# Optimization experiments

Hardware: AMD Instinct MI355X
Metric: run time of the kernel (lower is better)

The kernel has to match this reference:

```python
import jax, jax.numpy as jnp
import numpy as np

A, B, D, L = 256, 64, 768, 2  # annotators, batch, hidden, num_labels
G1, G2 = 4, 8                 # groups per attribute


def setup_inputs() -> dict:
    key = jax.random.key(0)
    ks = jax.random.split(key, 9)
    s = 1.0 / np.sqrt(D)
    return {
        "pooled": jax.random.normal(ks[0], (B, D), jnp.float32),
        "W1": jax.random.normal(ks[1], (G1, D, D), jnp.float32) * s,
        "b1": jax.random.normal(ks[2], (G1, D), jnp.float32) * s,
        "W2": jax.random.normal(ks[3], (G2, D, D), jnp.float32) * s,
        "b2": jax.random.normal(ks[4], (G2, D), jnp.float32) * s,
        "Wh": jax.random.normal(ks[5], (A, D, L), jnp.float32) * s,
        "bh": jax.random.normal(ks[6], (A, L), jnp.float32) * s,
        "g1_idx": jax.random.randint(ks[7], (A,), 0, G1),
        "g2_idx": jax.random.randint(ks[8], (A,), 0, G2),
    }


def reference(pooled, W1, b1, W2, b2, Wh, bh, g1_idx, g2_idx):
    # Attribute 1: every annotator with the same group shares the transform,
    # so compute once per group then gather (avoids A redundant GEMMs).
    h_g = jnp.einsum('bd,gde->gbe', pooled, W1) + b1[:, None, :]   # [G1, B, D]
    h = h_g[g1_idx]                                                # [A, B, D]
    # Attribute 2: input now differs per annotator -> grouped GEMM via gathered weights.
    h = jnp.einsum('abd,ade->abe', h, W2[g2_idx]) + b2[g2_idx][:, None, :]  # [A, B, D]
    # Per-annotator classification heads.
    logits = jnp.einsum('abd,adl->abl', h, Wh) + bh[:, None, :]    # [A, B, L]
    # Match torch layout: logits[batch, annotator, label]
    return jnp.transpose(logits, (1, 0, 2))                        # [B, A, L]
```

## Files before the change

kernel.cpp:

```cpp
#include <hip/hip_runtime.h>
#include <hip/hip_bf16.h>

#define AN 256
#define BN 64
#define DN 768
#define G1N 4
#define G2N 8
#define KI 24
#define LPAD 776

typedef __attribute__((ext_vector_type(8))) short short8;
typedef __attribute__((ext_vector_type(4))) short bf16x4;
typedef __attribute__((ext_vector_type(4))) float floatx4;

static __device__ __forceinline__ unsigned short f2bf(float f) {
    union { float f; unsigned int u; } v; v.f = f;
    unsigned int r = v.u + 0x7FFF + ((v.u >> 16) & 1);
    return (unsigned short)(r >> 16);
}
static __device__ __forceinline__ float bf2f(short s) {
    union { unsigned int u; float f; } v;
    v.u = ((unsigned int)(unsigned short)s) << 16;
    return v.f;
}

__global__ __launch_bounds__(256) void k_pack(
    const float* __restrict__ Wh, const float* __restrict__ b2,
    const float* __restrict__ bh, const int* __restrict__ g2i,
    unsigned short* __restrict__ Whp, float* __restrict__ bcu,
    int* __restrict__ s2idx)
{
    const int tid = threadIdx.x, a = blockIdx.x;
    __shared__ int g2s[AN];
    __shared__ int ss;
    g2s[tid] = g2i[tid];
    __syncthreads();
    if (tid == 0) {
        int my = g2s[a], s = 0;
        for (int j = 0; j < a; ++j) s += (g2s[j] == my);
        ss = s;
        s2idx[a] = s;
    }
    __syncthreads();
    const int my = g2s[a], s = ss;
    const size_t r0 = (size_t)my * 512 + 2 * s;
    const float* wa = Wh + (size_t)a * (DN * 2);

    #pragma unroll
    for (int i = 0; i < 3; ++i) {
        int e = i * 256 + tid;
        float2 v = *(const float2*)(wa + e * 2);
        Whp[r0 * DN + e]       = f2bf(v.x);
        Whp[(r0 + 1) * DN + e] = f2bf(v.y);
    }

    const int wave = tid >> 6, lane = tid & 63;
    if (wave < 2) {
        const int l = wave;
        const float* b2p = b2 + (size_t)my * DN;
        float sacc = 0.f;
        #pragma unroll
        for (int k = 0; k < 12; ++k) {
            int e = k * 64 + lane;
            sacc += wa[e * 2 + l] * b2p[e];
        }
        #pragma unroll
        for (int off = 1; off < 64; off <<= 1) sacc += __shfl_xor(sacc, off, 64);
        if (lane == 0) bcu[r0 + l] = sacc + bh[a * 2 + l];
    }
}

__global__ __launch_bounds__(256) void k_u(
    const float* __restrict__ W2, const unsigned short* __restrict__ Whp,
    const int* __restrict__ g2i, unsigned short* __restrict__ Wcs)
{
    const int g = blockIdx.y, d0 = blockIdx.x * 16;
    const int tid = threadIdx.x;
    const int n = __syncthreads_count(g2i[tid] == g);
    const int cols = 2 * n;
    const int nct = (cols + 15) >> 4;

    __shared__ unsigned short Bs[16 * LPAD];
    {
        const int srow = tid >> 4, t16 = tid & 15;
        const float* srcr = W2 + ((size_t)g * DN + d0 + srow) * DN;
        unsigned short* dstr = &Bs[srow * LPAD];
        #pragma unroll
        for (int i = 0; i < 12; ++i) {
            int col4 = (i * 16 + t16) * 4;
            float4 v = *(const float4*)(srcr + col4);
            bf16x4 b;
            b[0] = (short)f2bf(v.x); b[1] = (short)f2bf(v.y);
            b[2] = (short)f2bf(v.z); b[3] = (short)f2bf(v.w);
            *(bf16x4*)(dstr + col4) = b;
        }
    }
    __syncthreads();

    const int lane = tid & 63, wave = tid >> 6;
    const int nn = lane & 15, quad = lane >> 4;
    const unsigned short* bsp = &Bs[nn * LPAD + quad * 8];

    for (int ct = wave; ct < nct; ct += 4) {
        const int c = ct * 16 + nn;
        const int cl = (c < cols) ? c : cols - 1;
        const unsigned short* ap = Whp + ((size_t)g * 512 + cl) * DN + quad * 8;
        floatx4 acc = {0, 0, 0, 0};
        #pragma unroll
        for (int kk = 0; kk < KI; ++kk) {
            short8 af = *(const short8*)(ap + kk * 32);
            short8 bf = *(const short8*)(bsp + kk * 32);
            acc = __builtin_amdgcn_mfma_f32_16x16x32_bf16(af, bf, acc, 0, 0, 0);
        }
        #pragma unroll
        for (int r = 0; r < 4; ++r) {
            int cc = ct * 16 + quad * 4 + r;
            if (cc < cols)
                Wcs[((size_t)g * 512 + cc) * DN + d0 + nn] = f2bf(acc[r]);
        }
    }
}

__global__ __launch_bounds__(256) void k_v(
    const float* __restrict__ W1, const unsigned short* __restrict__ Wcs,
    const float* __restrict__ b1, const float* __restrict__ bcu,
    const int* __restrict__ g1i, const int* __restrict__ g2i,
    const int* __restrict__ s2idx,
    unsigned short* __restrict__ Vs, float* __restrict__ sv)
{
    const int g = blockIdx.y, d0 = blockIdx.x * 16;
    const int tid = threadIdx.x;
    __shared__ int g1s[AN];
    __shared__ int lst[AN];
    __shared__ int rpa[AN];
    g1s[tid] = g1i[tid];
    rpa[tid] = g2i[tid] * 512 + 2 * s2idx[tid];
    __syncthreads();
    int p1 = 0;
    const int m1 = g1s[tid];
    for (int a2 = 0; a2 < tid; ++a2) p1 += (g1s[a2] == m1);
    const int n = __syncthreads_count(m1 == g);
    if (m1 == g) lst[p1] = tid;
    const int cols = 2 * n;
    const int nct = (cols + 15) >> 4;

    __shared__ unsigned short Bs[16 * LPAD];
    {
        const int srow = tid >> 4, t16 = tid & 15;
        const float* srcr = W1 + ((size_t)g * DN + d0 + srow) * DN;
        unsigned short* dstr = &Bs[srow * LPAD];
        #pragma unroll
        for (int i = 0; i < 12; ++i) {
            int col4 = (i * 16 + t16) * 4;
            float4 v = *(const float4*)(srcr + col4);
            bf16x4 b;
            b[0] = (short)f2bf(v.x); b[1] = (short)f2bf(v.y);
            b[2] = (short)f2bf(v.z); b[3] = (short)f2bf(v.w);
            *(bf16x4*)(dstr + col4) = b;
        }
    }
    __syncthreads();

    const int lane = tid & 63, wave = tid >> 6;
    const int nn = lane & 15, quad = lane >> 4;
    const unsigned short* bsp = &Bs[nn * LPAD + quad * 8];
    const bool biasw = (blockIdx.x == 0);

    for (int ct = wave; ct < nct; ct += 4) {
        const int c = ct * 16 + nn;
        const int cl = (c < cols) ? c : cols - 1;
        const int a = lst[cl >> 1];
        const int rp = rpa[a] + (cl & 1);
        const unsigned short* ap = Wcs + (size_t)rp * DN + quad * 8;
        floatx4 acc = {0, 0, 0, 0};
        float sacc = 0.f;
        #pragma unroll
        for (int kk = 0; kk < KI; ++kk) {
            short8 af = *(const short8*)(ap + kk * 32);
            if (biasw) {
                const float* b1p = b1 + (size_t)g * DN + kk * 32 + quad * 8;
                float4 c0v = *(const float4*)(b1p);
                float4 c1v = *(const float4*)(b1p + 4);
                sacc += bf2f(af[0]) * c0v.x + bf2f(af[1]) * c0v.y
                      + bf2f(af[2]) * c0v.z + bf2f(af[3]) * c0v.w
                      + bf2f(af[4]) * c1v.x + bf2f(af[5]) * c1v.y
                      + bf2f(af[6]) * c1v.z + bf2f(af[7]) * c1v.w;
            }
            short8 bf = *(const short8*)(bsp + kk * 32);
            acc = __builtin_amdgcn_mfma_f32_16x16x32_bf16(af, bf, acc, 0, 0, 0);
        }
        #pragma unroll
        for (int r = 0; r < 4; ++r) {
            int cc = ct * 16 + quad * 4 + r;
            if (cc < cols)
                Vs[((size_t)g * 512 + cc) * DN + d0 + nn] = f2bf(acc[r]);
        }
        if (biasw) {
            sacc += __shfl_xor(sacc, 16, 64);
            sacc += __shfl_xor(sacc, 32, 64);
            if (quad == 0 && c < cols)
                sv[g * 512 + c] = sacc + bcu[rp];
        }
    }
}

__global__ __launch_bounds__(256) void k_out(
    const float* __restrict__ pooled, const unsigned short* __restrict__ Vs,
    const float* __restrict__ sv, const int* __restrict__ g1i,
    float* __restrict__ out)
{
    const int g = blockIdx.y;
    const int tid = threadIdx.x;
    __shared__ int g1s[AN];
    __shared__ int lst[AN];
    g1s[tid] = g1i[tid];
    __syncthreads();
    int p1 = 0;
    const int m1 = g1s[tid];
    for (int a2 = 0; a2 < tid; ++a2) p1 += (g1s[a2] == m1);
    const int n = __syncthreads_count(m1 == g);
    if (m1 == g) lst[p1] = tid;
    __syncthreads();
    const int cols = 2 * n;
    const int nt0 = blockIdx.x * 16;
    if (nt0 >= cols) return;

    const int lane = tid & 63, wave = tid >> 6;
    const int nn = lane & 15, quad = lane >> 4;

    const int c = nt0 + nn;
    const bool valid = (c < cols);
    const int cl = valid ? c : cols - 1;
    const int a = lst[cl >> 1], l = cl & 1;

    const float* ap = pooled + (size_t)(wave * 16 + nn) * DN + quad * 8;
    const unsigned short* bp = Vs + (size_t)(g * 512 + cl) * DN + quad * 8;

    floatx4 acc = {0, 0, 0, 0};
    #pragma unroll
    for (int kk = 0; kk < KI; ++kk) {
        float4 a0 = *(const float4*)(ap + kk * 32);
        float4 a1 = *(const float4*)(ap + kk * 32 + 4);
        short8 af;
        af[0] = (short)f2bf(a0.x); af[1] = (short)f2bf(a0.y);
        af[2] = (short)f2bf(a0.z); af[3] = (short)f2bf(a0.w);
        af[4] = (short)f2bf(a1.x); af[5] = (short)f2bf(a1.y);
        af[6] = (short)f2bf(a1.z); af[7] = (short)f2bf(a1.w);
        short8 bf = *(const short8*)(bp + kk * 32);
        acc = __builtin_amdgcn_mfma_f32_16x16x32_bf16(af, bf, acc, 0, 0, 0);
    }
    if (valid) {
        const float bv = sv[g * 512 + cl];
        #pragma unroll
        for (int r = 0; r < 4; ++r)
            out[(size_t)(wave * 16 + quad * 4 + r) * (AN * 2) + a * 2 + l] = acc[r] + bv;
    }
}

extern "C" void kernel_launch(void* const* d_in, const int* in_sizes, int n_in,
                              void* d_out, int out_size, void* d_ws, size_t ws_size,
                              hipStream_t stream) {
    const float* pooled = (const float*)d_in[0];
    const float* W1     = (const float*)d_in[1];
    const float* b1     = (const float*)d_in[2];
    const float* W2     = (const float*)d_in[3];
    const float* b2     = (const float*)d_in[4];
    const float* Wh     = (const float*)d_in[5];
    const float* bh     = (const float*)d_in[6];
    const int*   g1i    = (const int*)d_in[7];
    const int*   g2i    = (const int*)d_in[8];
    float* out = (float*)d_out;

    char* ws = (char*)d_ws;
    float* bcu   = (float*)ws;                  ws += (size_t)G2N * 512 * 4;
    float* sv    = (float*)ws;                  ws += (size_t)G1N * 512 * 4;
    int*   s2idx = (int*)ws;                    ws += (size_t)AN * 4;
    unsigned short* Whp = (unsigned short*)ws;  ws += (size_t)G2N * 512 * DN * 2;
    unsigned short* Wcs = (unsigned short*)ws;  ws += (size_t)G2N * 512 * DN * 2;
    unsigned short* Vs  = (unsigned short*)ws;  ws += (size_t)G1N * 512 * DN * 2;

    dim3 blk(256);
    k_pack<<<dim3(AN),        blk, 0, stream>>>(Wh, b2, bh, g2i, Whp, bcu, s2idx);
    k_u   <<<dim3(48, G2N),   blk, 0, stream>>>(W2, Whp, g2i, Wcs);
    k_v   <<<dim3(48, G1N),   blk, 0, stream>>>(W1, Wcs, b1, bcu, g1i, g2i, s2idx, Vs, sv);
    k_out <<<dim3(32, G1N),   blk, 0, stream>>>(pooled, Vs, sv, g1i, out);
}
```

Measured before the change: 138.1 us.

## Fuse four stage kernels into one persistent kernel with grid barriers

Merges the pack, W2-product, W1-product and output kernels into a single persistent kernel of 384 blocks, separated by atomic-counter grid barriers. A small init kernel resets the counters. This removes three inter-kernel launch gaps and drains. In exchange it relies on all blocks being co-resident, and adds spin-wait barrier overhead and idle blocks in the phases with smaller grids.

```diff
diff --git a/kernel.cpp b/kernel.cpp
--- a/kernel.cpp
+++ b/kernel.cpp
@@ -8,6 +8,7 @@
 #define G2N 8
 #define KI 24
 #define LPAD 776
+#define GRID 384
 
 typedef __attribute__((ext_vector_type(8))) short short8;
 typedef __attribute__((ext_vector_type(4))) short bf16x4;
@@ -24,236 +25,230 @@
     return v.f;
 }
 
-__global__ __launch_bounds__(256) void k_pack(
-    const float* __restrict__ Wh, const float* __restrict__ b2,
-    const float* __restrict__ bh, const int* __restrict__ g2i,
-    unsigned short* __restrict__ Whp, float* __restrict__ bcu,
-    int* __restrict__ s2idx)
+static __device__ __forceinline__ void grid_barrier(unsigned* ctr, unsigned target) {
+    __syncthreads();
+    if (threadIdx.x == 0) {
+        __threadfence();
+        atomicAdd(ctr, 1u);
+        while (__hip_atomic_load(ctr, __ATOMIC_RELAXED, __HIP_MEMORY_SCOPE_AGENT) < target)
+            __builtin_amdgcn_s_sleep(2);
+        __threadfence();
+    }
+    __syncthreads();
+}
+
+__global__ __launch_bounds__(64) void k_init(unsigned* __restrict__ ctr) {
+    if (threadIdx.x < 4) ctr[threadIdx.x] = 0u;
+}
+
+__global__ __launch_bounds__(256, 2) void k_fused(
+    const float* __restrict__ pooled, const float* __restrict__ W1,
+    const float* __restrict__ b1, const float* __restrict__ W2,
+    const float* __restrict__ b2, const float* __restrict__ Wh,
+    const float* __restrict__ bh, const int* __restrict__ g1i,
+    const int* __restrict__ g2i,
+    unsigned* __restrict__ ctr, float* __restrict__ bcu,
+    float* __restrict__ sv, int* __restrict__ s2idx,
+    unsigned short* __restrict__ Whp, unsigned short* __restrict__ Wcs,
+    unsigned short* __restrict__ Vs, float* __restrict__ out)
 {
-    const int tid = threadIdx.x, a = blockIdx.x;
-    __shared__ int g2s[AN];
-    __shared__ int ss;
-    g2s[tid] = g2i[tid];
-    __syncthreads();
-    if (tid == 0) {
-        int my = g2s[a], s = 0;
-        for (int j = 0; j < a; ++j) s += (g2s[j] == my);
-        ss = s;
-        s2idx[a] = s;
-    }
-    __syncthreads();
-    const int my = g2s[a], s = ss;
-    const size_t r0 = (size_t)my * 512 + 2 * s;
-    const float* wa = Wh + (size_t)a * (DN * 2);
-
-    #pragma unroll
-    for (int i = 0; i < 3; ++i) {
-        int e = i * 256 + tid;
-        float2 v = *(const float2*)(wa + e * 2);
-        Whp[r0 * DN + e]       = f2bf(v.x);
-        Whp[(r0 + 1) * DN + e] = f2bf(v.y);
-    }
-
-    const int wave = tid >> 6, lane = tid & 63;
-    if (wave < 2) {
-        const int l = wave;
-        const float* b2p = b2 + (size_t)my * DN;
-        float sacc = 0.f;
-        #pragma unroll
-        for (int k = 0; k < 12; ++k) {
-            int e = k * 64 + lane;
-            sacc += wa[e * 2 + l] * b2p[e];
-        }
-        #pragma unroll
-        for (int off = 1; off < 64; off <<= 1) sacc += __shfl_xor(sacc, off, 64);
-        if (lane == 0) bcu[r0 + l] = sacc + bh[a * 2 + l];
-    }
-}
-
-__global__ __launch_bounds__(256) void k_u(
-    const float* __restrict__ W2, const unsigned short* __restrict__ Whp,
-    const int* __restrict__ g2i, unsigned short* __restrict__ Wcs)
-{
-    const int g = blockIdx.y, d0 = blockIdx.x * 16;
+    __shared__ unsigned short Bs[16 * LPAD];
+    __shared__ int arrA[AN];
+    __shared__ int arrB[AN];
+    __shared__ int arrC[AN];
+    __shared__ int sscalar;
+
+    const int bx = blockIdx.x;
     const int tid = threadIdx.x;
-    const int n = __syncthreads_count(g2i[tid] == g);
-    const int cols = 2 * n;
-    const int nct = (cols + 15) >> 4;
-
-    __shared__ unsigned short Bs[16 * LPAD];
-    {
-        const int srow = tid >> 4, t16 = tid & 15;
-        const float* srcr = W2 + ((size_t)g * DN + d0 + srow) * DN;
-        unsigned short* dstr = &Bs[srow * LPAD];
-        #pragma unroll
-        for (int i = 0; i < 12; ++i) {
-            int col4 = (i * 16 + t16) * 4;
-            float4 v = *(const float4*)(srcr + col4);
-            bf16x4 b;
-            b[0] = (short)f2bf(v.x); b[1] = (short)f2bf(v.y);
-            b[2] = (short)f2bf(v.z); b[3] = (short)f2bf(v.w);
-            *(bf16x4*)(dstr + col4) = b;
-        }
-    }
-    __syncthreads();
-
     const int lane = tid & 63, wave = tid >> 6;
     const int nn = lane & 15, quad = lane >> 4;
-    const unsigned short* bsp = &Bs[nn * LPAD + quad * 8];
-
-    for (int ct = wave; ct < nct; ct += 4) {
-        const int c = ct * 16 + nn;
-        const int cl = (c < cols) ? c : cols - 1;
-        const unsigned short* ap = Whp + ((size_t)g * 512 + cl) * DN + quad * 8;
-        floatx4 acc = {0, 0, 0, 0};
+
+    if (bx < 256) {
+        const int a = bx;
+        arrA[tid] = g2i[tid];
+        __syncthreads();
+        if (tid == 0) {
+            int my = arrA[a], s = 0;
+            for (int j = 0; j < a; ++j) s += (arrA[j] == my);
+            sscalar = s;
+            s2idx[a] = s;
+        }
+        __syncthreads();
+        const int my = arrA[a], s = sscalar;
+        const size_t r0 = (size_t)my * 512 + 2 * s;
+        const float* wa = Wh + (size_t)a * (DN * 2);
         #pragma unroll
-        for (int kk = 0; kk < KI; ++kk) {
-            short8 af = *(const short8*)(ap + kk * 32);
-            short8 bf = *(const short8*)(bsp + kk * 32);
-            acc = __builtin_amdgcn_mfma_f32_16x16x32_bf16(af, bf, acc, 0, 0, 0);
-        }
-        #pragma unroll
-        for (int r = 0; r < 4; ++r) {
-            int cc = ct * 16 + quad * 4 + r;
-            if (cc < cols)
-                Wcs[((size_t)g * 512 + cc) * DN + d0 + nn] = f2bf(acc[r]);
-        }
-    }
-}
-
-__global__ __launch_bounds__(256) void k_v(
-    const float* __restrict__ W1, const unsigned short* __restrict__ Wcs,
-    const float* __restrict__ b1, const float* __restrict__ bcu,
-    const int* __restrict__ g1i, const int* __restrict__ g2i,
-    const int* __restrict__ s2idx,
-    unsigned short* __restrict__ Vs, float* __restrict__ sv)
-{
-    const int g = blockIdx.y, d0 = blockIdx.x * 16;
-    const int tid = threadIdx.x;
-    __shared__ int g1s[AN];
-    __shared__ int lst[AN];
-    __shared__ int rpa[AN];
-    g1s[tid] = g1i[tid];
-    rpa[tid] = g2i[tid] * 512 + 2 * s2idx[tid];
-    __syncthreads();
-    int p1 = 0;
-    const int m1 = g1s[tid];
-    for (int a2 = 0; a2 < tid; ++a2) p1 += (g1s[a2] == m1);
-    const int n = __syncthreads_count(m1 == g);
-    if (m1 == g) lst[p1] = tid;
-    const int cols = 2 * n;
-    const int nct = (cols + 15) >> 4;
-
-    __shared__ unsigned short Bs[16 * LPAD];
+        for (int i = 0; i < 3; ++i) {
+            int e = i * 256 + tid;
+            float2 v = *(const float2*)(wa + e * 2);
+            Whp[r0 * DN + e]       = f2bf(v.x);
+            Whp[(r0 + 1) * DN + e] = f2bf(v.y);
+        }
+        if (wave < 2) {
+            const int l = wave;
+            const float* b2p = b2 + (size_t)my * DN;
+            float sacc = 0.f;
+            #pragma unroll
+            for (int k = 0; k < 12; ++k) {
+                int e = k * 64 + lane;
+                sacc += wa[e * 2 + l] * b2p[e];
+            }
+            #pragma unroll
+            for (int off = 1; off < 64; off <<= 1) sacc += __shfl_xor(sacc, off, 64);
+            if (lane == 0) bcu[r0 + l] = sacc + bh[a * 2 + l];
+        }
+    }
+    grid_barrier(ctr + 0, GRID);
+
     {
-        const int srow = tid >> 4, t16 = tid & 15;
-        const float* srcr = W1 + ((size_t)g * DN + d0 + srow) * DN;
-        unsigned short* dstr = &Bs[srow * LPAD];
-        #pragma unroll
-        for (int i = 0; i < 12; ++i) {
-            int col4 = (i * 16 + t16) * 4;
-            float4 v = *(const float4*)(srcr + col4);
-            bf16x4 b;
-            b[0] = (short)f2bf(v.x); b[1] = (short)f2bf(v.y);
-            b[2] = (short)f2bf(v.z); b[3] = (short)f2bf(v.w);
-            *(bf16x4*)(dstr + col4) = b;
-        }
-    }
-    __syncthreads();
-
-    const int lane = tid & 63, wave = tid >> 6;
-    const int nn = lane & 15, quad = lane >> 4;
-    const unsigned short* bsp = &Bs[nn * LPAD + quad * 8];
-    const bool biasw = (blockIdx.x == 0);
-
-    for (int ct = wave; ct < nct; ct += 4) {
-        const int c = ct * 16 + nn;
-        const int cl = (c < cols) ? c : cols - 1;
-        const int a = lst[cl >> 1];
-        const int rp = rpa[a] + (cl & 1);
-        const unsigned short* ap = Wcs + (size_t)rp * DN + quad * 8;
-        floatx4 acc = {0, 0, 0, 0};
-        float sacc = 0.f;
-        #pragma unroll
-        for (int kk = 0; kk < KI; ++kk) {
-            short8 af = *(const short8*)(ap + kk * 32);
+        const int g = bx / 48, d0 = (bx % 48) * 16;
+        const int n = __syncthreads_count(g2i[tid] == g);
+        const int cols = 2 * n;
+        const int nct = (cols + 15) >> 4;
+        {
+            const int srow = tid >> 4, t16 = tid & 15;
+            const float* srcr = W2 + ((size_t)g * DN + d0 + srow) * DN;
+            unsigned short* dstr = &Bs[srow * LPAD];
+            #pragma unroll
+            for (int i = 0; i < 12; ++i) {
+                int col4 = (i * 16 + t16) * 4;
+                float4 v = *(const float4*)(srcr + col4);
+                bf16x4 b;
+                b[0] = (short)f2bf(v.x); b[1] = (short)f2bf(v.y);
+                b[2] = (short)f2bf(v.z); b[3] = (short)f2bf(v.w);
+                *(bf16x4*)(dstr + col4) = b;
+            }
+        }
+        __syncthreads();
+        const unsigned short* bsp = &Bs[nn * LPAD + quad * 8];
+        for (int ct = wave; ct < nct; ct += 4) {
+            const int c = ct * 16 + nn;
+            const int cl = (c < cols) ? c : cols - 1;
+            const unsigned short* ap = Whp + ((size_t)g * 512 + cl) * DN + quad * 8;
+            floatx4 acc = {0, 0, 0, 0};
+            #pragma unroll
+            for (int kk = 0; kk < KI; ++kk) {
+                short8 af = *(const short8*)(ap + kk * 32);
+                short8 bf = *(const short8*)(bsp + kk * 32);
+                acc = __builtin_amdgcn_mfma_f32_16x16x32_bf16(af, bf, acc, 0, 0, 0);
+            }
+            #pragma unroll
+            for (int r = 0; r < 4; ++r) {
+                int cc = ct * 16 + quad * 4 + r;
+                if (cc < cols)
+                    Wcs[((size_t)g * 512 + cc) * DN + d0 + nn] = f2bf(acc[r]);
+            }
+        }
+    }
+    grid_barrier(ctr + 1, GRID);
+
+    if (bx < 192) {
+        const int g = bx / 48, d0 = (bx % 48) * 16;
+        arrA[tid] = g1i[tid];
+        arrC[tid] = g2i[tid] * 512 + 2 * s2idx[tid];
+        __syncthreads();
+        int p1 = 0;
+        const int m1 = arrA[tid];
+        for (int a2 = 0; a2 < tid; ++a2) p1 += (arrA[a2] == m1);
+        const int n = __syncthreads_count(m1 == g);
+        if (m1 == g) arrB[p1] = tid;
+        const int cols = 2 * n;
+        const int nct = (cols + 15) >> 4;
+        {
+            const int srow = tid >> 4, t16 = tid & 15;
+            const float* srcr = W1 + ((size_t)g * DN + d0 + srow) * DN;
+            unsigned short* dstr = &Bs[srow * LPAD];
+            #pragma unroll
+            for (int i = 0; i < 12; ++i) {
+                int col4 = (i * 16 + t16) * 4;
+                float4 v = *(const float4*)(srcr + col4);
+                bf16x4 b;
+                b[0] = (short)f2bf(v.x); b[1] = (short)f2bf(v.y);
+                b[2] = (short)f2bf(v.z); b[3] = (short)f2bf(v.w);
+                *(bf16x4*)(dstr + col4) = b;
+            }
+        }
+        __syncthreads();
+        const unsigned short* bsp = &Bs[nn * LPAD + quad * 8];
+        const bool biasw = ((bx % 48) == 0);
+        for (int ct = wave; ct < nct; ct += 4) {
+            const int c = ct * 16 + nn;
+            const int cl = (c < cols) ? c : cols - 1;
+            const int a = arrB[cl >> 1];
+            const int rp = arrC[a] + (cl & 1);
+            const unsigned short* ap = Wcs + (size_t)rp * DN + quad * 8;
+            floatx4 acc = {0, 0, 0, 0};
+            float sacc = 0.f;
+            #pragma unroll
+            for (int kk = 0; kk < KI; ++kk) {
+                short8 af = *(const short8*)(ap + kk * 32);
+                if (biasw) {
+                    const float* b1p = b1 + (size_t)g * DN + kk * 32 + quad * 8;
+                    float4 c0v = *(const float4*)(b1p);
+                    float4 c1v = *(const float4*)(b1p + 4);
+                    sacc += bf2f(af[0]) * c0v.x + bf2f(af[1]) * c0v.y
+                          + bf2f(af[2]) * c0v.z + bf2f(af[3]) * c0v.w
+                          + bf2f(af[4]) * c1v.x + bf2f(af[5]) * c1v.y
+                          + bf2f(af[6]) * c1v.z + bf2f(af[7]) * c1v.w;
+                }
+                short8 bf = *(const short8*)(bsp + kk * 32);
+                acc = __builtin_amdgcn_mfma_f32_16x16x32_bf16(af, bf, acc, 0, 0, 0);
+            }
+            #pragma unroll
+            for (int r = 0; r < 4; ++r) {
+                int cc = ct * 16 + quad * 4 + r;
+                if (cc < cols)
+                    Vs[((size_t)g * 512 + cc) * DN + d0 + nn] = f2bf(acc[r]);
+            }
             if (biasw) {
-                const float* b1p = b1 + (size_t)g * DN + kk * 32 + quad * 8;
-                float4 c0v = *(const float4*)(b1p);
-                float4 c1v = *(const float4*)(b1p + 4);
-                sacc += bf2f(af[0]) * c0v.x + bf2f(af[1]) * c0v.y
-                      + bf2f(af[2]) * c0v.z + bf2f(af[3]) * c0v.w
-                      + bf2f(af[4]) * c1v.x + bf2f(af[5]) * c1v.y
-                      + bf2f(af[6]) * c1v.z + bf2f(af[7]) * c1v.w;
-            }
-            short8 bf = *(const short8*)(bsp + kk * 32);
-            acc = __builtin_amdgcn_mfma_f32_16x16x32_bf16(af, bf, acc, 0, 0, 0);
-        }
-        #pragma unroll
-        for (int r = 0; r < 4; ++r) {
-            int cc = ct * 16 + quad * 4 + r;
-            if (cc < cols)
-                Vs[((size_t)g * 512 + cc) * DN + d0 + nn] = f2bf(acc[r]);
-        }
-        if (biasw) {
-            sacc += __shfl_xor(sacc, 16, 64);
-            sacc += __shfl_xor(sacc, 32, 64);
-            if (quad == 0 && c < cols)
-                sv[g * 512 + c] = sacc + bcu[rp];
-        }
-    }
-}
-
-__global__ __launch_bounds__(256) void k_out(
-    const float* __restrict__ pooled, const unsigned short* __restrict__ Vs,
-    const float* __restrict__ sv, const int* __restrict__ g1i,
-    float* __restrict__ out)
-{
-    const int g = blockIdx.y;
-    const int tid = threadIdx.x;
-    __shared__ int g1s[AN];
-    __shared__ int lst[AN];
-    g1s[tid] = g1i[tid];
-    __syncthreads();
-    int p1 = 0;
-    const int m1 = g1s[tid];
-    for (int a2 = 0; a2 < tid; ++a2) p1 += (g1s[a2] == m1);
-    const int n = __syncthreads_count(m1 == g);
-    if (m1 == g) lst[p1] = tid;
-    __syncthreads();
-    const int cols = 2 * n;
-    const int nt0 = blockIdx.x * 16;
-    if (nt0 >= cols) return;
-
-    const int lane = tid & 63, wave = tid >> 6;
-    const int nn = lane & 15, quad = lane >> 4;
-
-    const int c = nt0 + nn;
-    const bool valid = (c < cols);
-    const int cl = valid ? c : cols - 1;
-    const int a = lst[cl >> 1], l = cl & 1;
-
-    const float* ap = pooled + (size_t)(wave * 16 + nn) * DN + quad * 8;
-    const unsigned short* bp = Vs + (size_t)(g * 512 + cl) * DN + quad * 8;
-
-    floatx4 acc = {0, 0, 0, 0};
-    #pragma unroll
-    for (int kk = 0; kk < KI; ++kk) {
-        float4 a0 = *(const float4*)(ap + kk * 32);
-        float4 a1 = *(const float4*)(ap + kk * 32 + 4);
-        short8 af;
-        af[0] = (short)f2bf(a0.x); af[1] = (short)f2bf(a0.y);
-        af[2] = (short)f2bf(a0.z); af[3] = (short)f2bf(a0.w);
-        af[4] = (short)f2bf(a1.x); af[5] = (short)f2bf(a1.y);
-        af[6] = (short)f2bf(a1.z); af[7] = (short)f2bf(a1.w);
-        short8 bf = *(const short8*)(bp + kk * 32);
-        acc = __builtin_amdgcn_mfma_f32_16x16x32_bf16(af, bf, acc, 0, 0, 0);
-    }
-    if (valid) {
-        const float bv = sv[g * 512 + cl];
-        #pragma unroll
-        for (int r = 0; r < 4; ++r)
-            out[(size_t)(wave * 16 + quad * 4 + r) * (AN * 2) + a * 2 + l] = acc[r] + bv;
+                sacc += __shfl_xor(sacc, 16, 64);
+                sacc += __shfl_xor(sacc, 32, 64);
+                if (quad == 0 && c < cols)
+                    sv[g * 512 + c] = sacc + bcu[rp];
+            }
+        }
+    }
+    grid_barrier(ctr + 2, GRID);
+
+    if (bx < 128) {
+        const int g = bx / 32, x = bx % 32;
+        arrA[tid] = g1i[tid];
+        __syncthreads();
+        int p1 = 0;
+        const int m1 = arrA[tid];
+        for (int a2 = 0; a2 < tid; ++a2) p1 += (arrA[a2] == m1);
+        const int n = __syncthreads_count(m1 == g);
+        if (m1 == g) arrB[p1] = tid;
+        __syncthreads();
+        const int cols = 2 * n;
+        const int nt0 = x * 16;
+        if (nt0 < cols) {
+            const int c = nt0 + nn;
+            const bool valid = (c < cols);
+            const int cl = valid ? c : cols - 1;
+            const int a = arrB[cl >> 1], l = cl & 1;
+            const float* ap = pooled + (size_t)(wave * 16 + nn) * DN + quad * 8;
+            const unsigned short* bp = Vs + (size_t)(g * 512 + cl) * DN + quad * 8;
+            floatx4 acc = {0, 0, 0, 0};
+            #pragma unroll
+            for (int kk = 0; kk < KI; ++kk) {
+                float4 a0 = *(const float4*)(ap + kk * 32);
+                float4 a1 = *(const float4*)(ap + kk * 32 + 4);
+                short8 af;
+                af[0] = (short)f2bf(a0.x); af[1] = (short)f2bf(a0.y);
+                af[2] = (short)f2bf(a0.z); af[3] = (short)f2bf(a0.w);
+                af[4] = (short)f2bf(a1.x); af[5] = (short)f2bf(a1.y);
+                af[6] = (short)f2bf(a1.z); af[7] = (short)f2bf(a1.w);
+                short8 bf = *(const short8*)(bp + kk * 32);
+                acc = __builtin_amdgcn_mfma_f32_16x16x32_bf16(af, bf, acc, 0, 0, 0);
+            }
+            if (valid) {
+                const float bv = sv[g * 512 + cl];
+                #pragma unroll
+                for (int r = 0; r < 4; ++r)
+                    out[(size_t)(wave * 16 + quad * 4 + r) * (AN * 2) + a * 2 + l] = acc[r] + bv;
+            }
+        }
     }
 }
 
@@ -272,6 +267,7 @@
     float* out = (float*)d_out;
 
     char* ws = (char*)d_ws;
+    unsigned* ctr = (unsigned*)ws;              ws += 16;
     float* bcu   = (float*)ws;                  ws += (size_t)G2N * 512 * 4;
     float* sv    = (float*)ws;                  ws += (size_t)G1N * 512 * 4;
     int*   s2idx = (int*)ws;                    ws += (size_t)AN * 4;
@@ -279,9 +275,8 @@
     unsigned short* Wcs = (unsigned short*)ws;  ws += (size_t)G2N * 512 * DN * 2;
     unsigned short* Vs  = (unsigned short*)ws;  ws += (size_t)G1N * 512 * DN * 2;
 
-    dim3 blk(256);
-    k_pack<<<dim3(AN),        blk, 0, stream>>>(Wh, b2, bh, g2i, Whp, bcu, s2idx);
-    k_u   <<<dim3(48, G2N),   blk, 0, stream>>>(W2, Whp, g2i, Wcs);
-    k_v   <<<dim3(48, G1N),   blk, 0, stream>>>(W1, Wcs, b1, bcu, g1i, g2i, s2idx, Vs, sv);
-    k_out <<<dim3(32, G1N),   blk, 0, stream>>>(pooled, Vs, sv, g1i, out);
-}
+    k_init <<<dim3(1),    dim3(64),  0, stream>>>(ctr);
+    k_fused<<<dim3(GRID), dim3(256), 0, stream>>>(pooled, W1, b1, W2, b2, Wh, bh,
+                                                  g1i, g2i, ctr, bcu, sv, s2idx,
+                                                  Whp, Wcs, Vs, out);
+}
```

After: 231.7 us. 67.8% more time.
